# Kernel tuning notes

Hardware: AMD Instinct MI355X
Metric: run time of the kernel (lower is better)

## Reference

```python
import jax, jax.numpy as jnp
import numpy as np

DIM = 1024
HEADS = 16
HEAD_DIM = DIM // HEADS
B, S = 2, 2048


def setup_inputs() -> dict:
    key = jax.random.key(0)
    ks = jax.random.split(key, 12)
    scale = 1.0 / np.sqrt(DIM)
    inp = {
        "Q_in": jax.random.normal(ks[0], (B, S, DIM), jnp.float32),
        "K_in": jax.random.normal(ks[1], (B, S, DIM), jnp.float32),
        "V_in": jax.random.normal(ks[2], (B, S, DIM), jnp.float32),
        "Wq": jax.random.normal(ks[3], (DIM, DIM), jnp.float32) * scale,
        "bq": jnp.zeros((DIM,), jnp.float32),
        "Wk": jax.random.normal(ks[4], (DIM, DIM), jnp.float32) * scale,
        "bk": jnp.zeros((DIM,), jnp.float32),
        "Wv": jax.random.normal(ks[5], (DIM, DIM), jnp.float32) * scale,
        "bv": jnp.zeros((DIM,), jnp.float32),
        "Wo": jax.random.normal(ks[6], (DIM, DIM), jnp.float32) * scale,
        "bo": jnp.zeros((DIM,), jnp.float32),
        "is_causal": 1,
    }
    return inp


def reference(Q_in, K_in, V_in, Wq, bq, Wk, bk, Wv, bv, Wo, bo, is_causal):
    b, s, d = Q_in.shape
    hd = d // HEADS
    # linear projections (torch nn.Linear: x @ W.T + b), split heads -> [b,h,s,hd]
    Q = (Q_in @ Wq.T + bq).reshape(b, s, HEADS, hd).transpose(0, 2, 1, 3)
    K = (K_in @ Wk.T + bk).reshape(b, s, HEADS, hd).transpose(0, 2, 1, 3)
    V = (V_in @ Wv.T + bv).reshape(b, s, HEADS, hd).transpose(0, 2, 1, 3)
    # full [b,h,s,s] score matrix, as in the original (no fused SDPA)
    scores = jnp.einsum("bhqd,bhkd->bhqk", Q, K) / jnp.sqrt(jnp.float32(hd))
    if is_causal:
        causal = jnp.tril(jnp.ones((s, s), dtype=bool))  # [s,s]
        scores = jnp.where(causal, scores, jnp.float32(-jnp.inf))
    attn = jax.nn.softmax(scores, axis=-1)
    # dropout is identity (eval mode) for a deterministic reference
    out = jnp.einsum("bhqk,bhkd->bhqd", attn, V)
    out = out.transpose(0, 2, 1, 3).reshape(b, s, d)
    return out @ Wo.T + bo
```

## Files before the change

### kernel.cpp

```cpp
#include <hip/hip_runtime.h>
#include <hip/hip_bf16.h>
#include <stdint.h>

#define HEADS 16
#define HD 64
#define BATCH 2
#define SEQ 2048
#define NDIM 1024
#define MROWS (BATCH * SEQ)

typedef __attribute__((ext_vector_type(8))) __bf16 bf16x8;
typedef __attribute__((ext_vector_type(4))) __bf16 bf16x4;
typedef __attribute__((ext_vector_type(4))) float f32x4;

#define LOG2E 1.4426950408889634f
#define SOFTMAX_C 16.0f

#if __has_builtin(__builtin_amdgcn_exp2f)
#define EXP2(x) __builtin_amdgcn_exp2f(x)
#else
#define EXP2(x) exp2f(x)
#endif

#define GLDS16(g, l)                                                          \
  __builtin_amdgcn_global_load_lds(                                           \
      (const __attribute__((address_space(1))) unsigned int*)(g),             \
      (__attribute__((address_space(3))) unsigned int*)(l), 16, 0, 0)

__global__ void cvt_w_kernel(const float* __restrict__ wq, const float* __restrict__ wk,
                             const float* __restrict__ wv, const float* __restrict__ wo,
                             __bf16* __restrict__ owq, __bf16* __restrict__ owk,
                             __bf16* __restrict__ owv, __bf16* __restrict__ owo) {
  const int id = blockIdx.x;
  const int m = id >> 10;
  const int blk = id & 1023;
  const float* in = (m == 0) ? wq : (m == 1) ? wk : (m == 2) ? wv : wo;
  __bf16* out = (m == 0) ? owq : (m == 1) ? owk : (m == 2) ? owv : owo;
  const size_t i = ((size_t)blk * 256 + threadIdx.x) * 4;
  const float4 v = *(const float4*)(in + i);
  bf16x4 o = {(__bf16)v.x, (__bf16)v.y, (__bf16)v.z, (__bf16)v.w};
  *(bf16x4*)(out + i) = o;
}

template <int BNF, bool TRC, bool AF32>
__device__ __forceinline__ void gemm_core(const void* __restrict__ Araw,
                                          const __bf16* __restrict__ B,
                                          int m0, int n0,
                                          char* lA, char* lB,
                                          f32x4 acc[4][BNF]) {
  constexpr int BBUF = BNF * 2048;
  const int t = threadIdx.x;
  const int lane = t & 63;
  const int llo = lane & 15, lhi = lane >> 4;
  const int wid = t >> 6;
  const int wrow = (wid >> 1) * 64;
  const int wcol = (wid & 1) * (BNF * 16);

  const int sl = (t & 7) ^ ((t >> 3) & 7);
  const int srg = 2 * (t >> 3) + (sl >> 2);
  const int cg = (sl & 3) * 8;

  const __bf16* pB0 = B + (size_t)(n0 + srg) * 1024 + cg;
  const __bf16* pB1 = B + (size_t)(n0 + (BNF == 4 ? 64 : 0) + srg) * 1024 + cg;

#pragma unroll
  for (int mf = 0; mf < 4; ++mf)
#pragma unroll
    for (int nf = 0; nf < BNF; ++nf)
      acc[mf][nf] = (f32x4){0.f, 0.f, 0.f, 0.f};

  const int fcol = ((((llo & 1) << 2) | lhi) ^ (llo >> 1)) << 4;

#define DSREAD_MFMA                                                           \
  do {                                                                        \
    bf16x8 af[4], bfr[BNF];                                                   \
    _Pragma("unroll")                                                         \
    for (int mf = 0; mf < 4; ++mf) {                                          \
      const int R = wrow + mf * 16 + llo;                                     \
      af[mf] = *(const bf16x8*)(lA + cb * 8192 + (R >> 1) * 128 + fcol);      \
    }                                                                         \
    _Pragma("unroll")                                                         \
    for (int nf = 0; nf < BNF; ++nf) {                                        \
      const int R = wcol + nf * 16 + llo;                                     \
      bfr[nf] = *(const bf16x8*)(lB + cb * BBUF + (R >> 1) * 128 + fcol);     \
    }                                                                         \
    __builtin_amdgcn_s_setprio(1);                                            \
    _Pragma("unroll")                                                         \
    for (int mf = 0; mf < 4; ++mf)                                            \
      _Pragma("unroll")                                                       \
      for (int nf = 0; nf < BNF; ++nf)                                        \
        acc[mf][nf] = TRC                                                     \
            ? __builtin_amdgcn_mfma_f32_16x16x32_bf16(bfr[nf], af[mf],        \
                                                      acc[mf][nf], 0, 0, 0)   \
            : __builtin_amdgcn_mfma_f32_16x16x32_bf16(af[mf], bfr[nf],        \
                                                      acc[mf][nf], 0, 0, 0);  \
    __builtin_amdgcn_s_setprio(0);                                            \
  } while (0)

  if constexpr (!AF32) {
    const __bf16* A = (const __bf16*)Araw;
    constexpr int NLD = (BNF == 4) ? 4 : 3;
    const __bf16* pA0 = A + (size_t)(m0 + srg) * 1024 + cg;
    const __bf16* pA1 = A + (size_t)(m0 + 64 + srg) * 1024 + cg;

#define STAGE_G(buf, k0)                                                      \
  do {                                                                        \
    GLDS16(pA0 + (k0), lA + (buf) * 8192 + t * 16);                           \
    GLDS16(pA1 + (k0), lA + (buf) * 8192 + 4096 + t * 16);                    \
    GLDS16(pB0 + (k0), lB + (buf) * BBUF + t * 16);                           \
    if (BNF == 4) GLDS16(pB1 + (k0), lB + (buf) * BBUF + 4096 + t * 16);      \
  } while (0)

    STAGE_G(0, 0);
    STAGE_G(1, 32);

    int cb = 0;
    for (int k0 = 0; k0 < 1024; k0 += 32) {
      const int step = k0 >> 5;
      if (step + 2 < 32) {
        const int sb = (cb >= 1) ? (cb - 1) : (cb + 2);
        STAGE_G(sb, k0 + 64);
        asm volatile("s_waitcnt vmcnt(%0)" :: "i"(2 * NLD) : "memory");
      } else if (step + 1 < 32) {
        asm volatile("s_waitcnt vmcnt(%0)" :: "i"(NLD) : "memory");
      } else {
        asm volatile("s_waitcnt vmcnt(0)" ::: "memory");
      }
      __builtin_amdgcn_s_barrier();
      __builtin_amdgcn_sched_barrier(0);
      DSREAD_MFMA;
      __builtin_amdgcn_s_barrier();
      cb = (cb == 2) ? 0 : (cb + 1);
    }
#undef STAGE_G
  } else {
    const float* fA = (const float*)Araw;
    const float* fpA0 = fA + (size_t)(m0 + srg) * 1024 + cg;
    const float* fpA1 = fA + (size_t)(m0 + 64 + srg) * 1024 + cg;

#define STAGEB(buf, k0)                                                       \
  do {                                                                        \
    GLDS16(pB0 + (k0), lB + (buf) * BBUF + t * 16);                           \
    if (BNF == 4) GLDS16(pB1 + (k0), lB + (buf) * BBUF + 4096 + t * 16);      \
  } while (0)

#define WRITEA(buf, sa, sb_, sc, sd)                                          \
  do {                                                                        \
    bf16x8 v0, v1;                                                            \
    v0[0]=(__bf16)(sa).x; v0[1]=(__bf16)(sa).y; v0[2]=(__bf16)(sa).z; v0[3]=(__bf16)(sa).w; \
    v0[4]=(__bf16)(sb_).x; v0[5]=(__bf16)(sb_).y; v0[6]=(__bf16)(sb_).z; v0[7]=(__bf16)(sb_).w; \
    v1[0]=(__bf16)(sc).x; v1[1]=(__bf16)(sc).y; v1[2]=(__bf16)(sc).z; v1[3]=(__bf16)(sc).w; \
    v1[4]=(__bf16)(sd).x; v1[5]=(__bf16)(sd).y; v1[6]=(__bf16)(sd).z; v1[7]=(__bf16)(sd).w; \
    *(bf16x8*)(lA + (buf) * 8192 + t * 16) = v0;                              \
    *(bf16x8*)(lA + (buf) * 8192 + 4096 + t * 16) = v1;                       \
  } while (0)

    float4 p0a, p0b, p0c, p0d;
    float4 p1a, p1b, p1c, p1d;

    p0a = *(const float4*)(fpA0 + 0);  p0b = *(const float4*)(fpA0 + 4);
    p0c = *(const float4*)(fpA1 + 0);  p0d = *(const float4*)(fpA1 + 4);
    WRITEA(0, p0a, p0b, p0c, p0d);
    STAGEB(0, 0);
    STAGEB(1, 32);
    p1a = *(const float4*)(fpA0 + 32); p1b = *(const float4*)(fpA0 + 36);
    p1c = *(const float4*)(fpA1 + 32); p1d = *(const float4*)(fpA1 + 36);

    int cb = 0;

#define QSTEP(K0CUR, LA_, LB_, LC_, LD_, WA_, WB_, WC_, WD_)                  \
  {                                                                           \
    const int step_ = (K0CUR) >> 5;                                           \
    const int wb_ = (cb == 2) ? 0 : cb + 1;                                   \
    const int sb_ = (wb_ == 2) ? 0 : wb_ + 1;                                 \
    if (step_ + 2 < 32) {                                                     \
      STAGEB(sb_, (K0CUR) + 64);                                              \
      LA_ = *(const float4*)(fpA0 + (K0CUR) + 64);                            \
      LB_ = *(const float4*)(fpA0 + (K0CUR) + 68);                            \
      LC_ = *(const float4*)(fpA1 + (K0CUR) + 64);                            \
      LD_ = *(const float4*)(fpA1 + (K0CUR) + 68);                            \
    }                                                                         \
    if (step_ + 1 < 32) WRITEA(wb_, WA_, WB_, WC_, WD_);                      \
    if (step_ + 2 < 32) {                                                     \
      asm volatile("s_waitcnt vmcnt(6)" ::: "memory");                        \
    } else {                                                                  \
      asm volatile("s_waitcnt vmcnt(0)" ::: "memory");                        \
    }                                                                         \
    asm volatile("s_waitcnt lgkmcnt(0)" ::: "memory");                        \
    __builtin_amdgcn_s_barrier();                                             \
    __builtin_amdgcn_sched_barrier(0);                                        \
    DSREAD_MFMA;                                                              \
    __builtin_amdgcn_s_barrier();                                             \
    cb = (cb == 2) ? 0 : (cb + 1);                                            \
  }

    for (int k0 = 0; k0 < 1024; k0 += 64) {
      QSTEP(k0,      p0a, p0b, p0c, p0d,  p1a, p1b, p1c, p1d);
      QSTEP(k0 + 32, p1a, p1b, p1c, p1d,  p0a, p0b, p0c, p0d);
    }
#undef QSTEP
#undef WRITEA
#undef STAGEB
  }
#undef DSREAD_MFMA
}

__global__ __launch_bounds__(256, 3)
void qkv_gemm_kernel(const float* __restrict__ Xq, const float* __restrict__ Xk,
                     const float* __restrict__ Xv, const __bf16* __restrict__ Wq,
                     const __bf16* __restrict__ Wk, const __bf16* __restrict__ Wv,
                     const float* __restrict__ bq, const float* __restrict__ bk,
                     const float* __restrict__ bv, __bf16* __restrict__ Qh,
                     __bf16* __restrict__ Kh, __bf16* __restrict__ Vt) {
  __shared__ __align__(16) char ldsA[3 * 8192];
  __shared__ __align__(16) char ldsB[3 * 8192];

  const int lid = blockIdx.x;
  const int xcd = lid & 7, slot = lid >> 3;
  const int y = slot >> 2;
  const int m0 = (xcd * 4 + (slot & 3)) * 128;
  const int mat = y >> 3;
  const int n0 = (y & 7) * 128;

  const void* A = (mat == 0) ? (const void*)Xq
                 : (mat == 1) ? (const void*)Xk : (const void*)Xv;
  const __bf16* B = (mat == 0) ? Wq : (mat == 1) ? Wk : Wv;
  const float* bias = (mat == 0) ? bq : (mat == 1) ? bk : bv;

  const int t = threadIdx.x;
  const int lane = t & 63;
  const int llo = lane & 15, lhi = lane >> 4;
  const int wid = t >> 6;
  const int wrow = (wid >> 1) * 64;
  const int wcol = (wid & 1) * 64;

  f32x4 acc[4][4];
  if (mat < 2) {
    gemm_core<4, true, true>(A, B, m0, n0, ldsA, ldsB, acc);
    __bf16* dst = (mat == 0) ? Qh : Kh;
    const float qs = (mat == 0) ? (0.125f * LOG2E) : 1.0f;
#pragma unroll
    for (int nf = 0; nf < 4; ++nf) {
      const int cbase = n0 + wcol + nf * 16 + lhi * 4;
      const float4 b4 = *(const float4*)(bias + cbase);
      const int h = cbase >> 6, d0 = cbase & 63;
#pragma unroll
      for (int mf = 0; mf < 4; ++mf) {
        const int sg = m0 + wrow + mf * 16 + llo;
        const int b = sg >> 11, s0 = sg & 2047;
        bf16x4 pk;
        pk[0] = (__bf16)((acc[mf][nf][0] + b4.x) * qs);
        pk[1] = (__bf16)((acc[mf][nf][1] + b4.y) * qs);
        pk[2] = (__bf16)((acc[mf][nf][2] + b4.z) * qs);
        pk[3] = (__bf16)((acc[mf][nf][3] + b4.w) * qs);
        *(bf16x4*)(dst + ((size_t)(b * HEADS + h) * SEQ + s0) * HD + d0) = pk;
      }
    }
  } else {
    gemm_core<4, false, true>(A, B, m0, n0, ldsA, ldsB, acc);
#pragma unroll
    for (int nf = 0; nf < 4; ++nf) {
      const int cfull = n0 + wcol + nf * 16 + llo;
      const int h = cfull >> 6, d = cfull & 63;
      const float bb = bias[cfull];
#pragma unroll
      for (int mf = 0; mf < 4; ++mf) {
        const int row0 = m0 + wrow + mf * 16 + lhi * 4;
        const int b = row0 >> 11;
        const int s0 = row0 & 2047;
        bf16x4 pk;
#pragma unroll
        for (int j = 0; j < 4; ++j) pk[j] = (__bf16)(acc[mf][nf][j] + bb);
        *(bf16x4*)(Vt + ((size_t)(b * HEADS + h) * HD + d) * SEQ + s0) = pk;
      }
    }
  }
}

__global__ __launch_bounds__(256, 4)
void attn_kernel(const __bf16* __restrict__ Qh, const __bf16* __restrict__ Kh,
                 const __bf16* __restrict__ Vt, __bf16* __restrict__ O,
                 const int* __restrict__ causal_flag) {
  __shared__ __align__(16) __bf16 kbuf[2][64 * 64];
  __shared__ __align__(16) __bf16 vbuf[2][64 * 64];
  __shared__ __align__(16) __bf16 pbuf[4][16 * 64];

  const int t = threadIdx.x;
  const int lane = t & 63;
  const int llo = lane & 15, lhi = lane >> 4;
  const int w = t >> 6;
  const int causal = causal_flag[0];

  const int lid = blockIdx.x;
  const int xcd = lid & 7, slot = lid >> 3;
  const int group = slot >> 5, r = slot & 31;
  const int bh = xcd + 8 * group;
  const int b = bh >> 4, h = bh & 15;
  const int rr = (group >= 2) ? ((r + 8) & 31) : r;
  const int qt = (group & 1) ? (31 - rr) : rr;

  const __bf16* Qb = Qh + (size_t)bh * SEQ * HD;
  const __bf16* Kb = Kh + (size_t)bh * SEQ * HD;
  const __bf16* Vb = Vt + (size_t)bh * HD * SEQ;

  const int sr = t >> 3;
  const int sce = (((t & 7) * 16) ^ ((sr & 7) << 4)) >> 1;
  const int swz = (llo & 7) << 4;

  char* const pw = (char*)&pbuf[w][0];

  const int qw = qt * 64 + w * 16;
  const int nt = causal ? (qt + 1) : (SEQ / 64);

  bf16x8 bQ[2];
#pragma unroll
  for (int ks = 0; ks < 2; ++ks)
    bQ[ks] = *(const bf16x8*)(Qb + (size_t)(qw + llo) * HD + ks * 32 + lhi * 8);

  float lrun = 0.f;
  f32x4 accO[4];
#pragma unroll
  for (int nf = 0; nf < 4; ++nf) accO[nf] = (f32x4){0.f, 0.f, 0.f, 0.f};

  GLDS16(Kb + (size_t)sr * HD + sce,        (char*)&kbuf[0][0] + t * 16);
  GLDS16(Kb + (size_t)(32 + sr) * HD + sce, (char*)&kbuf[0][0] + 4096 + t * 16);
  GLDS16(Vb + (size_t)sr * SEQ + sce,       (char*)&vbuf[0][0] + t * 16);
  GLDS16(Vb + (size_t)(32 + sr) * SEQ + sce,(char*)&vbuf[0][0] + 4096 + t * 16);
  int cur = 0;

  for (int tkv = 0; tkv < nt; ++tkv) {
    const bool hn = (tkv + 1 < nt);
    if (hn) {
      const int k0s = (tkv + 1) * 64;
      char* kd = (char*)&kbuf[cur ^ 1][0];
      char* vd = (char*)&vbuf[cur ^ 1][0];
      GLDS16(Kb + (size_t)(k0s + sr) * HD + sce,        kd + t * 16);
      GLDS16(Kb + (size_t)(k0s + 32 + sr) * HD + sce,   kd + 4096 + t * 16);
      GLDS16(Vb + (size_t)sr * SEQ + k0s + sce,         vd + t * 16);
      GLDS16(Vb + (size_t)(32 + sr) * SEQ + k0s + sce,  vd + 4096 + t * 16);
      asm volatile("s_waitcnt vmcnt(4)" ::: "memory");
    } else {
      asm volatile("s_waitcnt vmcnt(0)" ::: "memory");
    }
    __builtin_amdgcn_s_barrier();
    __builtin_amdgcn_sched_barrier(0);

    const int k0 = tkv * 64;
    const char* kb = (const char*)&kbuf[cur][0];
    const char* vb = (const char*)&vbuf[cur][0];

    f32x4 s[4];
#pragma unroll
    for (int nf = 0; nf < 4; ++nf) s[nf] = (f32x4){0.f, 0.f, 0.f, 0.f};
    __builtin_amdgcn_s_setprio(1);
#pragma unroll
    for (int ks = 0; ks < 2; ++ks)
#pragma unroll
      for (int nf = 0; nf < 4; ++nf) {
        bf16x8 aK = *(const bf16x8*)(kb + (nf * 16 + llo) * 128 +
                                     ((ks * 64 + lhi * 16) ^ swz));
        s[nf] = __builtin_amdgcn_mfma_f32_16x16x32_bf16(aK, bQ[ks], s[nf], 0, 0, 0);
      }
    __builtin_amdgcn_s_setprio(0);

    if (causal && tkv == qt) {
      const int qrow = qw + llo;
#pragma unroll
      for (int nf = 0; nf < 4; ++nf)
#pragma unroll
        for (int j = 0; j < 4; ++j)
          if (k0 + nf * 16 + lhi * 4 + j > qrow) s[nf][j] = -1e30f;
    }

#pragma unroll
    for (int nf = 0; nf < 4; ++nf)
#pragma unroll
      for (int j = 0; j < 4; ++j) {
        const float pv = EXP2(s[nf][j] - SOFTMAX_C);
        s[nf][j] = pv;
        lrun += pv;
      }

#pragma unroll
    for (int nf = 0; nf < 4; ++nf) {
      bf16x4 pk = {(__bf16)s[nf][0], (__bf16)s[nf][1], (__bf16)s[nf][2],
                   (__bf16)s[nf][3]};
      *(bf16x4*)(pw + llo * 128 + ((32 * nf + 8 * lhi) ^ swz)) = pk;
    }
    __builtin_amdgcn_s_setprio(1);
#pragma unroll
    for (int ks2 = 0; ks2 < 2; ++ks2) {
      bf16x8 bP = *(const bf16x8*)(pw + llo * 128 + ((64 * ks2 + 16 * lhi) ^ swz));
#pragma unroll
      for (int nf = 0; nf < 4; ++nf) {
        bf16x8 aV = *(const bf16x8*)(vb + (nf * 16 + llo) * 128 +
                                     ((64 * ks2 + 16 * lhi) ^ swz));
        accO[nf] = __builtin_amdgcn_mfma_f32_16x16x32_bf16(aV, bP, accO[nf], 0, 0, 0);
      }
    }
    __builtin_amdgcn_s_setprio(0);

    asm volatile("s_waitcnt lgkmcnt(0)" ::: "memory");
    __builtin_amdgcn_s_barrier();
    cur ^= 1;
  }

  lrun += __shfl_xor(lrun, 16, 64);
  lrun += __shfl_xor(lrun, 32, 64);
  const float linv = 1.f / lrun;
  const int srow = qw + llo;
#pragma unroll
  for (int nf = 0; nf < 4; ++nf) {
    bf16x4 pk;
#pragma unroll
    for (int j = 0; j < 4; ++j) pk[j] = (__bf16)(accO[nf][j] * linv);
    *(bf16x4*)(O + ((size_t)(b * SEQ + srow) * HEADS + h) * HD + nf * 16 +
               lhi * 4) = pk;
  }
}

__global__ __launch_bounds__(256, 4)
void out_gemm_kernel(const __bf16* __restrict__ Oin, const __bf16* __restrict__ Wo,
                     const float* __restrict__ bo, float* __restrict__ out) {
  __shared__ __align__(16) char ldsA[3 * 8192];
  __shared__ __align__(16) char ldsB[3 * 4096];

  const int lid = blockIdx.x;
  const int xcd = lid & 7, slot = lid >> 3;
  const int n0 = (slot >> 2) * 64;
  const int m0 = (xcd * 4 + (slot & 3)) * 128;

  f32x4 acc[4][2];
  gemm_core<2, false, false>((const void*)Oin, Wo, m0, n0, ldsA, ldsB, acc);

  const int t = threadIdx.x;
  const int lane = t & 63;
  const int llo = lane & 15, lhi = lane >> 4;
  const int wid = t >> 6;
  const int wrow = (wid >> 1) * 64;
  const int wcol = (wid & 1) * 32;

#pragma unroll
  for (int nf = 0; nf < 2; ++nf) {
    const int col = n0 + wcol + nf * 16 + llo;
    const float bb = bo[col];
#pragma unroll
    for (int mf = 0; mf < 4; ++mf)
#pragma unroll
      for (int j = 0; j < 4; ++j) {
        const int row = m0 + wrow + mf * 16 + lhi * 4 + j;
        out[(size_t)row * NDIM + col] = acc[mf][nf][j] + bb;
      }
  }
}

extern "C" void kernel_launch(void* const* d_in, const int* in_sizes, int n_in,
                              void* d_out, int out_size, void* d_ws, size_t ws_size,
                              hipStream_t stream) {
  const float* Q_in = (const float*)d_in[0];
  const float* K_in = (const float*)d_in[1];
  const float* V_in = (const float*)d_in[2];
  const float* Wq = (const float*)d_in[3];
  const float* bq = (const float*)d_in[4];
  const float* Wk = (const float*)d_in[5];
  const float* bk = (const float*)d_in[6];
  const float* Wv = (const float*)d_in[7];
  const float* bv = (const float*)d_in[8];
  const float* Wo = (const float*)d_in[9];
  const float* bo = (const float*)d_in[10];
  const int* causal = (const int*)d_in[11];
  float* out = (float*)d_out;

  char* p = (char*)d_ws;
  const size_t SZ_X = (size_t)MROWS * NDIM * 2;
  const size_t SZ_W = (size_t)NDIM * NDIM * 2;
  __bf16* bWq = (__bf16*)p; p += SZ_W;
  __bf16* bWk = (__bf16*)p; p += SZ_W;
  __bf16* bWv = (__bf16*)p; p += SZ_W;
  __bf16* bWo = (__bf16*)p; p += SZ_W;
  __bf16* Qh  = (__bf16*)p; p += SZ_X;
  __bf16* Kh  = (__bf16*)p; p += SZ_X;
  __bf16* Vt  = (__bf16*)p; p += SZ_X;
  __bf16* Obf = (__bf16*)p; p += SZ_X;

  cvt_w_kernel<<<4096, 256, 0, stream>>>(Wq, Wk, Wv, Wo, bWq, bWk, bWv, bWo);

  qkv_gemm_kernel<<<768, 256, 0, stream>>>(Q_in, K_in, V_in, bWq, bWk, bWv,
                                           bq, bk, bv, Qh, Kh, Vt);
  attn_kernel<<<1024, 256, 0, stream>>>(Qh, Kh, Vt, Obf, causal);
  out_gemm_kernel<<<512, 256, 0, stream>>>(Obf, bWo, bo, out);
}
```

Before: 107.6 us.

## Load fp32 A operand straight into MFMA registers, bypassing LDS staging

```diff
diff --git a/kernel.cpp b/kernel.cpp
--- a/kernel.cpp
+++ b/kernel.cpp
@@ -71,13 +71,105 @@
 
   const int fcol = ((((llo & 1) << 2) | lhi) ^ (llo >> 1)) << 4;
 
-#define DSREAD_MFMA                                                           \
+  if constexpr (!AF32) {
+    const __bf16* A = (const __bf16*)Araw;
+    constexpr int NLD = (BNF == 4) ? 4 : 3;
+    const __bf16* pA0 = A + (size_t)(m0 + srg) * 1024 + cg;
+    const __bf16* pA1 = A + (size_t)(m0 + 64 + srg) * 1024 + cg;
+
+#define STAGE_G(buf, k0)                                                      \
+  do {                                                                        \
+    GLDS16(pA0 + (k0), lA + (buf) * 8192 + t * 16);                           \
+    GLDS16(pA1 + (k0), lA + (buf) * 8192 + 4096 + t * 16);                    \
+    GLDS16(pB0 + (k0), lB + (buf) * BBUF + t * 16);                           \
+    if (BNF == 4) GLDS16(pB1 + (k0), lB + (buf) * BBUF + 4096 + t * 16);      \
+  } while (0)
+
+    STAGE_G(0, 0);
+    STAGE_G(1, 32);
+
+    int cb = 0;
+    for (int k0 = 0; k0 < 1024; k0 += 32) {
+      const int step = k0 >> 5;
+      if (step + 2 < 32) {
+        const int sb = (cb >= 1) ? (cb - 1) : (cb + 2);
+        STAGE_G(sb, k0 + 64);
+        asm volatile("s_waitcnt vmcnt(%0)" :: "i"(2 * NLD) : "memory");
+      } else if (step + 1 < 32) {
+        asm volatile("s_waitcnt vmcnt(%0)" :: "i"(NLD) : "memory");
+      } else {
+        asm volatile("s_waitcnt vmcnt(0)" ::: "memory");
+      }
+      __builtin_amdgcn_s_barrier();
+      __builtin_amdgcn_sched_barrier(0);
+      {
+        bf16x8 af[4], bfr[BNF];
+#pragma unroll
+        for (int mf = 0; mf < 4; ++mf) {
+          const int R = wrow + mf * 16 + llo;
+          af[mf] = *(const bf16x8*)(lA + cb * 8192 + (R >> 1) * 128 + fcol);
+        }
+#pragma unroll
+        for (int nf = 0; nf < BNF; ++nf) {
+          const int R = wcol + nf * 16 + llo;
+          bfr[nf] = *(const bf16x8*)(lB + cb * BBUF + (R >> 1) * 128 + fcol);
+        }
+        __builtin_amdgcn_s_setprio(1);
+#pragma unroll
+        for (int mf = 0; mf < 4; ++mf)
+#pragma unroll
+          for (int nf = 0; nf < BNF; ++nf)
+            acc[mf][nf] = TRC
+                ? __builtin_amdgcn_mfma_f32_16x16x32_bf16(bfr[nf], af[mf],
+                                                          acc[mf][nf], 0, 0, 0)
+                : __builtin_amdgcn_mfma_f32_16x16x32_bf16(af[mf], bfr[nf],
+                                                          acc[mf][nf], 0, 0, 0);
+        __builtin_amdgcn_s_setprio(0);
+      }
+      __builtin_amdgcn_s_barrier();
+      cb = (cb == 2) ? 0 : (cb + 1);
+    }
+#undef STAGE_G
+  } else {
+    const float* fA = (const float*)Araw;
+    const float* aB0 = fA + (size_t)(m0 + wrow +  0 + llo) * 1024 + lhi * 8;
+    const float* aB1 = fA + (size_t)(m0 + wrow + 16 + llo) * 1024 + lhi * 8;
+    const float* aB2 = fA + (size_t)(m0 + wrow + 32 + llo) * 1024 + lhi * 8;
+    const float* aB3 = fA + (size_t)(m0 + wrow + 48 + llo) * 1024 + lhi * 8;
+
+    float4 as[2][4][2];
+
+#define STAGEB(buf, k0)                                                       \
+  do {                                                                        \
+    GLDS16(pB0 + (k0), lB + (buf) * BBUF + t * 16);                           \
+    if (BNF == 4) GLDS16(pB1 + (k0), lB + (buf) * BBUF + 4096 + t * 16);      \
+  } while (0)
+
+#define LOADA(ph, k0)                                                         \
+  do {                                                                        \
+    as[ph][0][0] = *(const float4*)(aB0 + (k0));                              \
+    as[ph][0][1] = *(const float4*)(aB0 + (k0) + 4);                          \
+    as[ph][1][0] = *(const float4*)(aB1 + (k0));                              \
+    as[ph][1][1] = *(const float4*)(aB1 + (k0) + 4);                          \
+    as[ph][2][0] = *(const float4*)(aB2 + (k0));                              \
+    as[ph][2][1] = *(const float4*)(aB2 + (k0) + 4);                          \
+    as[ph][3][0] = *(const float4*)(aB3 + (k0));                              \
+    as[ph][3][1] = *(const float4*)(aB3 + (k0) + 4);                          \
+  } while (0)
+
+#define CVTMFMA(ph)                                                           \
   do {                                                                        \
     bf16x8 af[4], bfr[BNF];                                                   \
     _Pragma("unroll")                                                         \
     for (int mf = 0; mf < 4; ++mf) {                                          \
-      const int R = wrow + mf * 16 + llo;                                     \
-      af[mf] = *(const bf16x8*)(lA + cb * 8192 + (R >> 1) * 128 + fcol);      \
+      af[mf][0] = (__bf16)as[ph][mf][0].x;                                    \
+      af[mf][1] = (__bf16)as[ph][mf][0].y;                                    \
+      af[mf][2] = (__bf16)as[ph][mf][0].z;                                    \
+      af[mf][3] = (__bf16)as[ph][mf][0].w;                                    \
+      af[mf][4] = (__bf16)as[ph][mf][1].x;                                    \
+      af[mf][5] = (__bf16)as[ph][mf][1].y;                                    \
+      af[mf][6] = (__bf16)as[ph][mf][1].z;                                    \
+      af[mf][7] = (__bf16)as[ph][mf][1].w;                                    \
     }                                                                         \
     _Pragma("unroll")                                                         \
     for (int nf = 0; nf < BNF; ++nf) {                                        \
@@ -97,112 +189,42 @@
     __builtin_amdgcn_s_setprio(0);                                            \
   } while (0)
 
-  if constexpr (!AF32) {
-    const __bf16* A = (const __bf16*)Araw;
-    constexpr int NLD = (BNF == 4) ? 4 : 3;
-    const __bf16* pA0 = A + (size_t)(m0 + srg) * 1024 + cg;
-    const __bf16* pA1 = A + (size_t)(m0 + 64 + srg) * 1024 + cg;
-
-#define STAGE_G(buf, k0)                                                      \
-  do {                                                                        \
-    GLDS16(pA0 + (k0), lA + (buf) * 8192 + t * 16);                           \
-    GLDS16(pA1 + (k0), lA + (buf) * 8192 + 4096 + t * 16);                    \
-    GLDS16(pB0 + (k0), lB + (buf) * BBUF + t * 16);                           \
-    if (BNF == 4) GLDS16(pB1 + (k0), lB + (buf) * BBUF + 4096 + t * 16);      \
-  } while (0)
-
-    STAGE_G(0, 0);
-    STAGE_G(1, 32);
-
-    int cb = 0;
-    for (int k0 = 0; k0 < 1024; k0 += 32) {
-      const int step = k0 >> 5;
-      if (step + 2 < 32) {
-        const int sb = (cb >= 1) ? (cb - 1) : (cb + 2);
-        STAGE_G(sb, k0 + 64);
-        asm volatile("s_waitcnt vmcnt(%0)" :: "i"(2 * NLD) : "memory");
-      } else if (step + 1 < 32) {
-        asm volatile("s_waitcnt vmcnt(%0)" :: "i"(NLD) : "memory");
-      } else {
-        asm volatile("s_waitcnt vmcnt(0)" ::: "memory");
-      }
-      __builtin_amdgcn_s_barrier();
-      __builtin_amdgcn_sched_barrier(0);
-      DSREAD_MFMA;
-      __builtin_amdgcn_s_barrier();
-      cb = (cb == 2) ? 0 : (cb + 1);
-    }
-#undef STAGE_G
-  } else {
-    const float* fA = (const float*)Araw;
-    const float* fpA0 = fA + (size_t)(m0 + srg) * 1024 + cg;
-    const float* fpA1 = fA + (size_t)(m0 + 64 + srg) * 1024 + cg;
-
-#define STAGEB(buf, k0)                                                       \
-  do {                                                                        \
-    GLDS16(pB0 + (k0), lB + (buf) * BBUF + t * 16);                           \
-    if (BNF == 4) GLDS16(pB1 + (k0), lB + (buf) * BBUF + 4096 + t * 16);      \
-  } while (0)
-
-#define WRITEA(buf, sa, sb_, sc, sd)                                          \
-  do {                                                                        \
-    bf16x8 v0, v1;                                                            \
-    v0[0]=(__bf16)(sa).x; v0[1]=(__bf16)(sa).y; v0[2]=(__bf16)(sa).z; v0[3]=(__bf16)(sa).w; \
-    v0[4]=(__bf16)(sb_).x; v0[5]=(__bf16)(sb_).y; v0[6]=(__bf16)(sb_).z; v0[7]=(__bf16)(sb_).w; \
-    v1[0]=(__bf16)(sc).x; v1[1]=(__bf16)(sc).y; v1[2]=(__bf16)(sc).z; v1[3]=(__bf16)(sc).w; \
-    v1[4]=(__bf16)(sd).x; v1[5]=(__bf16)(sd).y; v1[6]=(__bf16)(sd).z; v1[7]=(__bf16)(sd).w; \
-    *(bf16x8*)(lA + (buf) * 8192 + t * 16) = v0;                              \
-    *(bf16x8*)(lA + (buf) * 8192 + 4096 + t * 16) = v1;                       \
-  } while (0)
-
-    float4 p0a, p0b, p0c, p0d;
-    float4 p1a, p1b, p1c, p1d;
-
-    p0a = *(const float4*)(fpA0 + 0);  p0b = *(const float4*)(fpA0 + 4);
-    p0c = *(const float4*)(fpA1 + 0);  p0d = *(const float4*)(fpA1 + 4);
-    WRITEA(0, p0a, p0b, p0c, p0d);
+    LOADA(0, 0);
     STAGEB(0, 0);
     STAGEB(1, 32);
-    p1a = *(const float4*)(fpA0 + 32); p1b = *(const float4*)(fpA0 + 36);
-    p1c = *(const float4*)(fpA1 + 32); p1d = *(const float4*)(fpA1 + 36);
 
     int cb = 0;
-
-#define QSTEP(K0CUR, LA_, LB_, LC_, LD_, WA_, WB_, WC_, WD_)                  \
+#define QSTEPD(K0CUR, PH, PHN)                                                \
   {                                                                           \
     const int step_ = (K0CUR) >> 5;                                           \
-    const int wb_ = (cb == 2) ? 0 : cb + 1;                                   \
-    const int sb_ = (wb_ == 2) ? 0 : wb_ + 1;                                 \
-    if (step_ + 2 < 32) {                                                     \
-      STAGEB(sb_, (K0CUR) + 64);                                              \
-      LA_ = *(const float4*)(fpA0 + (K0CUR) + 64);                            \
-      LB_ = *(const float4*)(fpA0 + (K0CUR) + 68);                            \
-      LC_ = *(const float4*)(fpA1 + (K0CUR) + 64);                            \
-      LD_ = *(const float4*)(fpA1 + (K0CUR) + 68);                            \
-    }                                                                         \
-    if (step_ + 1 < 32) WRITEA(wb_, WA_, WB_, WC_, WD_);                      \
-    if (step_ + 2 < 32) {                                                     \
-      asm volatile("s_waitcnt vmcnt(6)" ::: "memory");                        \
+    const int sb_ = (cb == 0) ? 2 : cb - 1;                     \
+    if (step_ + 2 < 32) STAGEB(sb_, (K0CUR) + 64);                            \
+    if (step_ + 1 < 32) LOADA(PHN, (K0CUR) + 32);                             \
+    if (step_ < 2) {                                                          \
+      asm volatile("s_waitcnt vmcnt(12)" ::: "memory");                       \
+    } else if (step_ < 30) {                                                  \
+      asm volatile("s_waitcnt vmcnt(28)" ::: "memory");                       \
+    } else if (step_ == 30) {                                                 \
+      asm volatile("s_waitcnt vmcnt(16)" ::: "memory");                       \
     } else {                                                                  \
       asm volatile("s_waitcnt vmcnt(0)" ::: "memory");                        \
     }                                                                         \
-    asm volatile("s_waitcnt lgkmcnt(0)" ::: "memory");                        \
     __builtin_amdgcn_s_barrier();                                             \
     __builtin_amdgcn_sched_barrier(0);                                        \
-    DSREAD_MFMA;                                                              \
+    CVTMFMA(PH);                                                              \
     __builtin_amdgcn_s_barrier();                                             \
     cb = (cb == 2) ? 0 : (cb + 1);                                            \
   }
 
     for (int k0 = 0; k0 < 1024; k0 += 64) {
-      QSTEP(k0,      p0a, p0b, p0c, p0d,  p1a, p1b, p1c, p1d);
-      QSTEP(k0 + 32, p1a, p1b, p1c, p1d,  p0a, p0b, p0c, p0d);
-    }
-#undef QSTEP
-#undef WRITEA
+      QSTEPD(k0, 0, 1);
+      QSTEPD(k0 + 32, 1, 0);
+    }
+#undef QSTEPD
+#undef CVTMFMA
+#undef LOADA
 #undef STAGEB
   }
-#undef DSREAD_MFMA
 }
 
 __global__ __launch_bounds__(256, 3)
@@ -212,7 +234,6 @@
                      const float* __restrict__ bq, const float* __restrict__ bk,
                      const float* __restrict__ bv, __bf16* __restrict__ Qh,
                      __bf16* __restrict__ Kh, __bf16* __restrict__ Vt) {
-  __shared__ __align__(16) char ldsA[3 * 8192];
   __shared__ __align__(16) char ldsB[3 * 8192];
 
   const int lid = blockIdx.x;
@@ -236,7 +257,7 @@
 
   f32x4 acc[4][4];
   if (mat < 2) {
-    gemm_core<4, true, true>(A, B, m0, n0, ldsA, ldsB, acc);
+    gemm_core<4, true, true>(A, B, m0, n0, nullptr, ldsB, acc);
     __bf16* dst = (mat == 0) ? Qh : Kh;
     const float qs = (mat == 0) ? (0.125f * LOG2E) : 1.0f;
 #pragma unroll
@@ -257,7 +278,7 @@
       }
     }
   } else {
-    gemm_core<4, false, true>(A, B, m0, n0, ldsA, ldsB, acc);
+    gemm_core<4, false, true>(A, B, m0, n0, nullptr, ldsB, acc);
 #pragma unroll
     for (int nf = 0; nf < 4; ++nf) {
       const int cfull = n0 + wcol + nf * 16 + llo;
```

New measurement: 202.6 us. 88.2% more time.
